# Kernel optimization log

Hardware: AMD Instinct MI355X
Metric: run time of the kernel (lower is better)

The kernel has to match this reference:

```python
import jax, jax.numpy as jnp
import numpy as np

EPS = 1e-6
BN_EPS = 1e-5


def _grid_idx(loc, Hg, Wg):
    # loc: [B, N0, 2] in [-1, 1], (x, y) order -> nearest cell index in Hg x Wg grid
    loc = jnp.clip(loc, -1.0, 1.0)
    px = jnp.clip(jnp.round(0.5 * (loc[..., 0] + 1.0) * Wg - 0.5).astype(jnp.int32), 0, Wg - 1)
    py = jnp.clip(jnp.round(0.5 * (loc[..., 1] + 1.0) * Hg - 0.5).astype(jnp.int32), 0, Hg - 1)
    return py * Wg + px  # [B, N0]


def token2map(x, loc_orig, idx_agg, H, W):
    # scatter-average token features into an H x W map via the original points
    B, N, C = x.shape
    idx_hw = _grid_idx(loc_orig, H, W)                         # [B, N0]
    feat = jnp.take_along_axis(x, idx_agg[..., None], axis=1)  # [B, N0, C]
    ssum = jax.vmap(lambda s, i, f: s.at[i].add(f))(jnp.zeros((B, H * W, C), x.dtype), idx_hw, feat)
    cnt = jax.vmap(lambda c, i: c.at[i].add(1.0))(jnp.zeros((B, H * W), x.dtype), idx_hw)
    return (ssum / (cnt[..., None] + EPS)).reshape(B, H, W, C)


def map2token(x_map, N, loc_orig, idx_agg, agg_weight):
    # bilinear gather from map at original points, then weighted scatter-mean to N tokens
    B, Hd, Wd, C = x_map.shape
    loc = jnp.clip(loc_orig, -1.0, 1.0)
    fx = jnp.clip(0.5 * (loc[..., 0] + 1.0) * Wd - 0.5, 0.0, Wd - 1.0)
    fy = jnp.clip(0.5 * (loc[..., 1] + 1.0) * Hd - 0.5, 0.0, Hd - 1.0)
    x0 = jnp.floor(fx); y0 = jnp.floor(fy)
    wx = fx - x0; wy = fy - y0
    x0i = x0.astype(jnp.int32); y0i = y0.astype(jnp.int32)
    x1i = jnp.minimum(x0i + 1, Wd - 1); y1i = jnp.minimum(y0i + 1, Hd - 1)
    mp = x_map.reshape(B, Hd * Wd, C)
    g = lambda iy, ix: jnp.take_along_axis(mp, (iy * Wd + ix)[..., None], axis=1)  # [B, N0, C]
    f = (((1 - wx) * (1 - wy))[..., None] * g(y0i, x0i)
         + (wx * (1 - wy))[..., None] * g(y0i, x1i)
         + ((1 - wx) * wy)[..., None] * g(y1i, x0i)
         + (wx * wy)[..., None] * g(y1i, x1i))
    wpt = agg_weight[..., 0]                                   # [B, N0]
    num = jax.vmap(lambda n, i, s: n.at[i].add(s))(jnp.zeros((B, N, C), f.dtype), idx_agg, f * wpt[..., None])
    den = jax.vmap(lambda d, i, w: d.at[i].add(w))(jnp.zeros((B, N), f.dtype), idx_agg, wpt)
    return num / (den[..., None] + EPS)


def token_cluster_grid(x, loc_orig, idx_agg, agg_weight, weight, Hc, Wc):
    # weighted merge of tokens into Hc x Wc coarse grid cells (keyed by original points)
    B, N, C = x.shape
    Ns = Hc * Wc
    idx_cell = _grid_idx(loc_orig, Hc, Wc)                     # [B, N0] -> new token id
    wtok = weight[..., 0]                                      # [B, N] token confidence weight
    wpt = jnp.take_along_axis(wtok, idx_agg, axis=1)           # [B, N0]
    fpt = jnp.take_along_axis(x, idx_agg[..., None], axis=1)   # [B, N0, C]
    num = jax.vmap(lambda n, i, s: n.at[i].add(s))(jnp.zeros((B, Ns, C), x.dtype), idx_cell, fpt * wpt[..., None])
    den = jax.vmap(lambda d, i, w: d.at[i].add(w))(jnp.zeros((B, Ns), x.dtype), idx_cell, wpt)
    x_down = num / (den[..., None] + EPS)
    weight_t = (wpt / (jnp.take_along_axis(den, idx_cell, axis=1) + EPS))[..., None]  # [B, N0, 1]
    agg_weight_down = agg_weight * weight_t
    agg_weight_down = agg_weight_down / jnp.max(agg_weight_down, axis=1, keepdims=True)
    return x_down, idx_cell, agg_weight_down


def setup_inputs() -> dict:
    key = jax.random.key(0)
    ks = jax.random.split(key, 8)
    B, N, C_in, C_out = 4, 16384, 128, 256
    H = W = 256
    N0 = H * W
    x = jax.random.normal(ks[0], (B, N, C_in), jnp.float32)
    loc_orig = jax.random.uniform(ks[1], (B, N0, 2), jnp.float32, -1.0, 1.0)
    idx_agg = jax.random.randint(ks[2], (B, N0), 0, N, jnp.int32)
    agg_weight = jax.random.uniform(ks[3], (B, N0, 1), jnp.float32)
    conv_w = jax.random.normal(ks[4], (3, 3, C_in, C_out), jnp.float32) / np.sqrt(9 * C_in).astype(np.float32)
    conv_b = jnp.zeros((C_out,), jnp.float32)
    skip_w = jax.random.normal(ks[5], (C_out, C_in), jnp.float32) / np.sqrt(C_in).astype(np.float32)
    bn_gamma = jnp.ones((C_out,), jnp.float32)
    bn_beta = jnp.zeros((C_out,), jnp.float32)
    conf_w = jax.random.normal(ks[6], (1, C_out), jnp.float32) / np.sqrt(C_out).astype(np.float32)
    conf_b = jnp.zeros((1,), jnp.float32)
    return {"x": x, "loc_orig": loc_orig, "idx_agg": idx_agg, "agg_weight": agg_weight,
            "conv_w": conv_w, "conv_b": conv_b, "skip_w": skip_w,
            "bn_gamma": bn_gamma, "bn_beta": bn_beta, "conf_w": conf_w, "conf_b": conf_b,
            "H": H, "W": W}


def reference(x, loc_orig, idx_agg, agg_weight, conv_w, conv_b, skip_w, bn_gamma, bn_beta, conf_w, conf_b, H, W):
    B, N, C = x.shape
    # scatter tokens to map, 3x3 s2 conv
    x_map = token2map(x, loc_orig, idx_agg, H, W)              # [B, H, W, C]
    y = jax.lax.conv_general_dilated(x_map, conv_w, (2, 2), ((1, 1), (1, 1)),
                                     dimension_numbers=("NHWC", "HWIO", "NHWC")) + conv_b
    Hd = (H - 1) // 2 + 1
    Wd = (W - 1) // 2 + 1
    # gather back to tokens + linear skip
    tok = map2token(y, N, loc_orig, idx_agg, agg_weight) + x @ skip_w.T   # [B, N, C_out]
    # BatchNorm2d over tokens (train-mode batch stats, per channel)
    mu = jnp.mean(tok, axis=(0, 1))
    var = jnp.var(tok, axis=(0, 1))
    tokn = (tok - mu) / jnp.sqrt(var + BN_EPS) * bn_gamma + bn_beta
    conf = tokn @ conf_w.T + conf_b                            # [B, N, 1]
    weight = jnp.exp(conf)
    # grid clustering: merge to (Hd//2) x (Wd//2) cells = N * sample_ratio tokens
    x_down, idx_agg_down, agg_weight_down = token_cluster_grid(tokn, loc_orig, idx_agg, agg_weight, weight, Hd // 2, Wd // 2)
    x_down = jax.nn.relu(x_down)
    x_out = jax.nn.relu(tokn)
    return x_down, x_out, conf, agg_weight_down, idx_agg_down
```

## Files before the change

kernel.cpp:

```cpp
#include <hip/hip_runtime.h>
#include <hip/hip_bf16.h>
#include <math.h>

#define BB    4
#define NTOK  16384
#define CIN   128
#define COUT  256
#define HM    256
#define WM    256
#define NP    65536
#define HD    128
#define WD    128
#define HC    64
#define WC    64
#define NS    4096
#define EPS   1e-6f
#define BNEPS 1e-5f

#define SEG_TOK  (BB * NP)
#define SEG_64   (SEG_TOK + BB * NTOK)
#define NSEG     (SEG_64 + BB * NS)

typedef __attribute__((ext_vector_type(8))) short bfrag8;
typedef __attribute__((ext_vector_type(4))) float ffrag4;

static constexpr size_t BNSUM_OFF  = 0;
static constexpr size_t BNSQ_OFF   = BNSUM_OFF + 256;
static constexpr size_t MAXW_OFF   = BNSQ_OFF + 256;
static constexpr size_t CNTS_OFF   = MAXW_OFF + 256;
static constexpr size_t CURS_OFF   = CNTS_OFF + NSEG;
static constexpr size_t ZERO_FLOATS = CURS_OFF + NSEG;
static constexpr size_t YBUF_OFF   = (ZERO_FLOATS + 255) & ~(size_t)255;
static constexpr size_t XMAPN_OFF  = YBUF_OFF + (size_t)BB * HD * WD * COUT / 2;
static constexpr size_t XBF_OFF    = XMAPN_OFF + (size_t)BB * NP * CIN / 2;
static constexpr size_t TOKB_OFF   = XBF_OFF + (size_t)BB * NTOK * CIN / 2;
static constexpr size_t WFRAG_OFF  = TOKB_OFF + (size_t)BB * NTOK * COUT / 2;
static constexpr size_t SFRAG_OFF  = WFRAG_OFF + (size_t)9 * 4 * 16 * 512 / 2;
static constexpr size_t WEXP_OFF   = SFRAG_OFF + (size_t)4 * 16 * 512 / 2;
static constexpr size_t AWDT_OFF   = WEXP_OFF + (size_t)BB * NTOK;
static constexpr size_t ABUF_OFF   = AWDT_OFF + (size_t)BB * NP;
static constexpr size_t BBUF_OFF   = ABUF_OFF + 256;
static constexpr size_t CWA_OFF    = BBUF_OFF + 256;
static constexpr size_t C0_OFF     = CWA_OFF + 256;
static constexpr size_t CELL256_OFF = C0_OFF + 256;
static constexpr size_t CELL64_OFF  = CELL256_OFF + (size_t)BB * NP;
static constexpr size_t DEN2_OFF   = CELL64_OFF + (size_t)BB * NP;
static constexpr size_t STARTS_OFF = DEN2_OFF + (size_t)BB * NS;
static constexpr size_t BLKSUM_OFF = STARTS_OFF + NSEG;
static constexpr size_t BLKEXCL_OFF = BLKSUM_OFF + 512;
static constexpr size_t PIDX_OFF   = BLKEXCL_OFF + 512;


__device__ __forceinline__ unsigned short f2bf(float f) {
    unsigned int u = __float_as_uint(f);
    return (unsigned short)((u + 0x7FFFu + ((u >> 16) & 1u)) >> 16);
}
__device__ __forceinline__ float bf2f(unsigned short u) {
    return __uint_as_float((unsigned int)u << 16);
}


__global__ void k_cellhist(const float* __restrict__ loc, const int* __restrict__ idx_agg,
                           int* __restrict__ cell256, int* __restrict__ cell64,
                           int* __restrict__ cnts) {
    int i = blockIdx.x * 256 + threadIdx.x;
    int b = i >> 16;
    float lx = fminf(fmaxf(loc[2 * (size_t)i], -1.f), 1.f);
    float ly = fminf(fmaxf(loc[2 * (size_t)i + 1], -1.f), 1.f);
    int px = (int)rintf(0.5f * (lx + 1.f) * WM - 0.5f);
    px = min(max(px, 0), WM - 1);
    int py = (int)rintf(0.5f * (ly + 1.f) * HM - 0.5f);
    py = min(max(py, 0), HM - 1);
    int c256 = py * WM + px;
    cell256[i] = c256;
    int qx = (int)rintf(0.5f * (lx + 1.f) * WC - 0.5f);
    qx = min(max(qx, 0), WC - 1);
    int qy = (int)rintf(0.5f * (ly + 1.f) * HC - 0.5f);
    qy = min(max(qy, 0), HC - 1);
    int c64 = qy * WC + qx;
    cell64[i] = c64;
    atomicAdd(&cnts[b * NP + c256], 1);
    atomicAdd(&cnts[SEG_TOK + b * NTOK + idx_agg[i]], 1);
    atomicAdd(&cnts[SEG_64 + b * NS + c64], 1);
}

__global__ void k_xcast(const float* __restrict__ x, unsigned short* __restrict__ xbf) {
    size_t i = (size_t)blockIdx.x * 256 + threadIdx.x;
    float4 v = ((const float4*)x)[i];
    ushort4 o;
    o.x = f2bf(v.x); o.y = f2bf(v.y); o.z = f2bf(v.z); o.w = f2bf(v.w);
    ((ushort4*)xbf)[i] = o;
}

__global__ __launch_bounds__(256) void k_scan1(const int* __restrict__ cnts,
                                               int* __restrict__ starts,
                                               int* __restrict__ blksum) {
    int t = threadIdx.x;
    int base = blockIdx.x * 1024 + t * 4;
    int4 v = *(const int4*)(cnts + base);
    int tsum = v.x + v.y + v.z + v.w;
    __shared__ int s[256];
    s[t] = tsum;
    __syncthreads();
    for (int off = 1; off < 256; off <<= 1) {
        int add = (t >= off) ? s[t - off] : 0;
        __syncthreads();
        s[t] += add;
        __syncthreads();
    }
    int excl = s[t] - tsum;
    int4 o;
    o.x = excl; o.y = excl + v.x; o.z = o.y + v.y; o.w = o.z + v.z;
    *(int4*)(starts + base) = o;
    if (t == 255) blksum[blockIdx.x] = s[255];
}

__global__ __launch_bounds__(512) void k_scan2(const int* __restrict__ blksum,
                                               int* __restrict__ blkexcl) {
    int t = threadIdx.x;
    __shared__ int s[512];
    int v = (t < 336) ? blksum[t] : 0;
    s[t] = v;
    __syncthreads();
    for (int off = 1; off < 512; off <<= 1) {
        int add = (t >= off) ? s[t - off] : 0;
        __syncthreads();
        s[t] += add;
        __syncthreads();
    }
    if (t < 336) blkexcl[t] = s[t] - v;
}

__global__ void k_fill(const int* __restrict__ cell256, const int* __restrict__ idx_agg,
                       const int* __restrict__ cell64, const int* __restrict__ starts,
                       const int* __restrict__ blkexcl, int* __restrict__ curs,
                       int* __restrict__ pidx) {
    int gp = blockIdx.x * 256 + threadIdx.x;
    int b = gp >> 16;
    int ia = idx_agg[gp];
    int t1 = b * NP + cell256[gp];
    int p1 = starts[t1] + blkexcl[t1 >> 10] + atomicAdd(&curs[t1], 1);
    pidx[p1] = ia;
    int t2 = SEG_TOK + b * NTOK + ia;
    int p2 = starts[t2] + blkexcl[t2 >> 10] + atomicAdd(&curs[t2], 1);
    pidx[p2] = gp;
    int t3 = SEG_64 + b * NS + cell64[gp];
    int p3 = starts[t3] + blkexcl[t3 >> 10] + atomicAdd(&curs[t3], 1);
    pidx[p3] = ia;
}

__global__ __launch_bounds__(256) void k_gather_map(const unsigned short* __restrict__ xbf,
                                                    const int* __restrict__ starts,
                                                    const int* __restrict__ blkexcl,
                                                    const int* __restrict__ cnts,
                                                    const int* __restrict__ pidx,
                                                    unsigned short* __restrict__ xmapn) {
    int tgt = blockIdx.x * 8 + (threadIdx.x >> 5);
    int lane = threadIdx.x & 31;
    int b = tgt >> 16;
    int start = starts[tgt] + blkexcl[tgt >> 10];
    int cnt = cnts[tgt];
    float4 acc = make_float4(0.f, 0.f, 0.f, 0.f);
    for (int j = 0; j < cnt; ++j) {
        int tk = pidx[start + j];
        ushort4 u = *(const ushort4*)(xbf + ((size_t)b * NTOK + tk) * CIN + lane * 4);
        acc.x += bf2f(u.x); acc.y += bf2f(u.y); acc.z += bf2f(u.z); acc.w += bf2f(u.w);
    }
    float inv = 1.0f / ((float)cnt + EPS);
    ushort4 o;
    o.x = f2bf(acc.x * inv);
    o.y = f2bf(acc.y * inv);
    o.z = f2bf(acc.z * inv);
    o.w = f2bf(acc.w * inv);
    *(ushort4*)(xmapn + (size_t)tgt * CIN + lane * 4) = o;
}

__global__ void k_wfrag(const float* __restrict__ cw, unsigned short* __restrict__ wfrag) {
    int i = blockIdx.x * 256 + threadIdx.x;
    int j = i & 7;
    int lane = (i >> 3) & 63;
    int nt = (i >> 9) & 15;
    int kc = (i >> 13) & 3;
    int khw = i >> 15;
    int c = kc * 32 + ((lane >> 4) << 3) + j;
    int n = nt * 16 + (lane & 15);
    wfrag[i] = f2bf(cw[((size_t)khw * CIN + c) * COUT + n]);
}

__global__ void k_sfrag(const float* __restrict__ sw, unsigned short* __restrict__ sfrag) {
    int i = blockIdx.x * 256 + threadIdx.x;
    int j = i & 7;
    int lane = (i >> 3) & 63;
    int nt = (i >> 9) & 15;
    int kc = i >> 13;
    int c = kc * 32 + ((lane >> 4) << 3) + j;
    int n = nt * 16 + (lane & 15);
    sfrag[i] = f2bf(sw[(size_t)n * CIN + c]);
}

__global__ __launch_bounds__(256) void k_convmf(const unsigned short* __restrict__ xmapn,
                                                const unsigned short* __restrict__ wfrag,
                                                const float* __restrict__ cb,
                                                unsigned short* __restrict__ y) {
    int bz = blockIdx.x;
    int ow0 = (bz & 1) * 64;
    int oh = (bz >> 1) & (HD - 1);
    int b = bz >> 8;
    int tid = threadIdx.x;
    int w = tid >> 6, lane = tid & 63;
    int n0 = w * 64;

    __shared__ unsigned short s_even[65 * 136];
    __shared__ unsigned short s_odd[64 * 136];

    ffrag4 acc[4][4];
#pragma unroll
    for (int mt = 0; mt < 4; ++mt)
#pragma unroll
        for (int nt = 0; nt < 4; ++nt) {
            ffrag4 z = {0.f, 0.f, 0.f, 0.f};
            acc[mt][nt] = z;
        }

    int iw0 = 2 * ow0 - 1;
    int lm = lane & 15;
    int lq = lane >> 4;
    int cbase = lq << 3;

    for (int kh = 0; kh < 3; ++kh) {
        int ih = 2 * oh - 1 + kh;
        __syncthreads();
        {
            const unsigned short* rowb =
                xmapn + ((size_t)b * NP + (size_t)ih * WM) * CIN;
            bool ihok = (ih >= 0 && ih < HM);
            for (int idx = tid; idx < 129 * 16; idx += 256) {
                int pix = idx >> 4;
                int c8 = (idx & 15) * 8;
                int iw = iw0 + pix;
                uint4 v = make_uint4(0u, 0u, 0u, 0u);
                if (ihok && iw >= 0 && iw < WM)
                    v = *(const uint4*)(rowb + (size_t)iw * CIN + c8);
                unsigned short* dst = (pix & 1)
                    ? &s_odd[(size_t)((pix - 1) >> 1) * 136 + c8]
                    : &s_even[(size_t)(pix >> 1) * 136 + c8];
                *(uint4*)dst = v;
            }
        }
        __syncthreads();
#pragma unroll
        for (int kw = 0; kw < 3; ++kw) {
            int khw = kh * 3 + kw;
#pragma unroll
            for (int kc = 0; kc < 4; ++kc) {
                int c = kc * 32 + cbase;
                bfrag8 af[4];
#pragma unroll
                for (int mt = 0; mt < 4; ++mt) {
                    int m = mt * 16 + lm;
                    const unsigned short* src;
                    if (kw == 1)      src = &s_odd[(size_t)m * 136 + c];
                    else if (kw == 0) src = &s_even[(size_t)m * 136 + c];
                    else              src = &s_even[(size_t)(m + 1) * 136 + c];
                    af[mt] = *(const bfrag8*)(const void*)src;
                }
                const unsigned short* wb =
                    wfrag + ((size_t)((khw * 4 + kc) * 16) + w * 4) * 512 + lane * 8;
#pragma unroll
                for (int nt = 0; nt < 4; ++nt) {
                    bfrag8 bf = *(const bfrag8*)(const void*)(wb + (size_t)nt * 512);
#pragma unroll
                    for (int mt = 0; mt < 4; ++mt)
                        acc[mt][nt] = __builtin_amdgcn_mfma_f32_16x16x32_bf16(
                            af[mt], bf, acc[mt][nt], 0, 0, 0);
                }
            }
        }
    }

    unsigned short* yb = y + (((size_t)b * HD + oh) * WD + ow0) * COUT;
#pragma unroll
    for (int nt = 0; nt < 4; ++nt) {
        int n = n0 + nt * 16 + lm;
        float bias = cb[n];
#pragma unroll
        for (int mt = 0; mt < 4; ++mt) {
#pragma unroll
            for (int r = 0; r < 4; ++r) {
                int m = mt * 16 + lq * 4 + r;
                yb[(size_t)m * COUT + n] = f2bf(acc[mt][nt][r] + bias);
            }
        }
    }
}

__global__ __launch_bounds__(256) void k_gtokmf(const unsigned short* __restrict__ y,
                                                const float* __restrict__ loc,
                                                const float* __restrict__ aggw,
                                                const unsigned short* __restrict__ xbf,
                                                const unsigned short* __restrict__ sfrag,
                                                const int* __restrict__ starts,
                                                const int* __restrict__ blkexcl,
                                                const int* __restrict__ cnts,
                                                const int* __restrict__ pidx,
                                                float* __restrict__ tok,
                                                float* __restrict__ bnsum,
                                                float* __restrict__ bnsq) {
    int t0 = blockIdx.x * 64;
    int tid = threadIdx.x;
    int w = tid >> 6, lane = tid & 63;
    __shared__ unsigned short s_num[64 * 264];

    for (int i = 0; i < 16; ++i) {
        int row = w * 16 + i;
        int tl = t0 + row;
        int b = tl >> 14;
        int tgt = SEG_TOK + tl;
        int start = starts[tgt] + blkexcl[tgt >> 10];
        int cnt = cnts[tgt];
        const unsigned short* ybase = y + (size_t)b * (HD * WD * COUT);
        float4 num = make_float4(0.f, 0.f, 0.f, 0.f);
        float den = 0.f;
        for (int j = 0; j < cnt; ++j) {
            int gp = pidx[start + j];
            float lx = fminf(fmaxf(loc[2 * (size_t)gp], -1.f), 1.f);
            float ly = fminf(fmaxf(loc[2 * (size_t)gp + 1], -1.f), 1.f);
            float fx = fminf(fmaxf(0.5f * (lx + 1.f) * WD - 0.5f, 0.f), (float)(WD - 1));
            float fy = fminf(fmaxf(0.5f * (ly + 1.f) * HD - 0.5f, 0.f), (float)(HD - 1));
            float x0f = floorf(fx), y0f = floorf(fy);
            float wx = fx - x0f, wy = fy - y0f;
            int x0 = (int)x0f, y0 = (int)y0f;
            int x1 = min(x0 + 1, WD - 1), y1 = min(y0 + 1, HD - 1);
            ushort4 u00 = *(const ushort4*)(ybase + ((size_t)y0 * WD + x0) * COUT + lane * 4);
            ushort4 u01 = *(const ushort4*)(ybase + ((size_t)y0 * WD + x1) * COUT + lane * 4);
            ushort4 u10 = *(const ushort4*)(ybase + ((size_t)y1 * WD + x0) * COUT + lane * 4);
            ushort4 u11 = *(const ushort4*)(ybase + ((size_t)y1 * WD + x1) * COUT + lane * 4);
            float w00 = (1.f - wx) * (1.f - wy), w01 = wx * (1.f - wy);
            float w10 = (1.f - wx) * wy, w11 = wx * wy;
            float aw = aggw[gp];
            num.x += (w00 * bf2f(u00.x) + w01 * bf2f(u01.x) + w10 * bf2f(u10.x) + w11 * bf2f(u11.x)) * aw;
            num.y += (w00 * bf2f(u00.y) + w01 * bf2f(u01.y) + w10 * bf2f(u10.y) + w11 * bf2f(u11.y)) * aw;
            num.z += (w00 * bf2f(u00.z) + w01 * bf2f(u01.z) + w10 * bf2f(u10.z) + w11 * bf2f(u11.z)) * aw;
            num.w += (w00 * bf2f(u00.w) + w01 * bf2f(u01.w) + w10 * bf2f(u10.w) + w11 * bf2f(u11.w)) * aw;
            den += aw;
        }
        float inv = 1.f / (den + EPS);
        ushort4 o;
        o.x = f2bf(num.x * inv);
        o.y = f2bf(num.y * inv);
        o.z = f2bf(num.z * inv);
        o.w = f2bf(num.w * inv);
        *(ushort4*)&s_num[(size_t)row * 264 + lane * 4] = o;
    }
    __syncthreads();

    int lm = lane & 15, lq = lane >> 4;
    int n0 = w * 64;
    ffrag4 acc[4][4];
#pragma unroll
    for (int mt = 0; mt < 4; ++mt)
#pragma unroll
        for (int nt = 0; nt < 4; ++nt) {
            ffrag4 z = {0.f, 0.f, 0.f, 0.f};
            acc[mt][nt] = z;
        }
#pragma unroll
    for (int kc = 0; kc < 4; ++kc) {
        bfrag8 af[4];
#pragma unroll
        for (int mt = 0; mt < 4; ++mt)
            af[mt] = *(const bfrag8*)(const void*)(xbf +
                     (size_t)(t0 + mt * 16 + lm) * CIN + kc * 32 + lq * 8);
        const unsigned short* sb = sfrag + ((size_t)(kc * 16) + w * 4) * 512 + lane * 8;
#pragma unroll
        for (int nt = 0; nt < 4; ++nt) {
            bfrag8 bf = *(const bfrag8*)(const void*)(sb + (size_t)nt * 512);
#pragma unroll
            for (int mt = 0; mt < 4; ++mt)
                acc[mt][nt] = __builtin_amdgcn_mfma_f32_16x16x32_bf16(
                    af[mt], bf, acc[mt][nt], 0, 0, 0);
        }
    }

    float bsum[4] = {0.f, 0.f, 0.f, 0.f};
    float bsq[4] = {0.f, 0.f, 0.f, 0.f};
#pragma unroll
    for (int mt = 0; mt < 4; ++mt) {
#pragma unroll
        for (int r = 0; r < 4; ++r) {
            int row = mt * 16 + lq * 4 + r;
            int tkn = t0 + row;
#pragma unroll
            for (int nt = 0; nt < 4; ++nt) {
                int n = n0 + nt * 16 + lm;
                float v = bf2f(s_num[(size_t)row * 264 + n]) + acc[mt][nt][r];
                tok[(size_t)tkn * COUT + n] = v;
                bsum[nt] += v;
                bsq[nt] = fmaf(v, v, bsq[nt]);
            }
        }
    }
#pragma unroll
    for (int nt = 0; nt < 4; ++nt) {
        bsum[nt] += __shfl_down(bsum[nt], 32);
        bsq[nt] += __shfl_down(bsq[nt], 32);
        bsum[nt] += __shfl_down(bsum[nt], 16);
        bsq[nt] += __shfl_down(bsq[nt], 16);
    }
    if (lq == 0) {
#pragma unroll
        for (int nt = 0; nt < 4; ++nt) {
            int n = n0 + nt * 16 + lm;
            atomicAdd(&bnsum[n], bsum[nt]);
            atomicAdd(&bnsq[n], bsq[nt]);
        }
    }
}

__global__ void k_bnparams(const float* __restrict__ bnsum, const float* __restrict__ bnsq,
                           const float* __restrict__ gamma, const float* __restrict__ beta,
                           const float* __restrict__ confw, const float* __restrict__ confb,
                           float* __restrict__ abuf, float* __restrict__ bbuf,
                           float* __restrict__ cwa, float* __restrict__ c0) {
    int k = threadIdx.x;
    const float cntv = (float)(BB * NTOK);
    float mu = bnsum[k] / cntv;
    float var = bnsq[k] / cntv - mu * mu;
    float a = gamma[k] * rsqrtf(var + BNEPS);
    float bbv = beta[k] - mu * a;
    abuf[k] = a;
    bbuf[k] = bbv;
    float cw = confw[k];
    cwa[k] = a * cw;
    __shared__ float red[256];
    red[k] = bbv * cw;
    __syncthreads();
    for (int s = 128; s > 0; s >>= 1) {
        if (k < s) red[k] += red[k + s];
        __syncthreads();
    }
    if (k == 0) c0[0] = red[0] + confb[0];
}

__global__ void k_confrelu(float* __restrict__ tok, const float* __restrict__ cwa,
                           const float* __restrict__ c0v, const float* __restrict__ abuf,
                           const float* __restrict__ bbuf, float* __restrict__ conf_out,
                           unsigned short* __restrict__ tokb, float* __restrict__ wexp) {
    int tid = threadIdx.x;
    int tkn = blockIdx.x * 16 + (tid >> 4);
    int kc = (tid & 15) * 16;
    float* row = tok + (size_t)tkn * COUT + kc;
    unsigned short* tb = tokb + (size_t)tkn * COUT + kc;
    float s = 0.f;
#pragma unroll
    for (int i = 0; i < 16; i += 4) {
        float4 v = *(const float4*)(row + i);
        float4 w = *(const float4*)(cwa + kc + i);
        float4 a = *(const float4*)(abuf + kc + i);
        float4 bb = *(const float4*)(bbuf + kc + i);
        s += v.x * w.x + v.y * w.y + v.z * w.z + v.w * w.w;
        float4 tn;
        tn.x = fmaf(a.x, v.x, bb.x);
        tn.y = fmaf(a.y, v.y, bb.y);
        tn.z = fmaf(a.z, v.z, bb.z);
        tn.w = fmaf(a.w, v.w, bb.w);
        ushort4 o;
        o.x = f2bf(tn.x); o.y = f2bf(tn.y); o.z = f2bf(tn.z); o.w = f2bf(tn.w);
        *(ushort4*)(tb + i) = o;
        float4 rl;
        rl.x = fmaxf(tn.x, 0.f); rl.y = fmaxf(tn.y, 0.f);
        rl.z = fmaxf(tn.z, 0.f); rl.w = fmaxf(tn.w, 0.f);
        *(float4*)(row + i) = rl;
    }
    for (int off = 8; off > 0; off >>= 1) s += __shfl_down(s, off, 16);
    if ((tid & 15) == 0) {
        float cv = s + c0v[0];
        conf_out[tkn] = cv;
        wexp[tkn] = expf(cv);
    }
}

__global__ __launch_bounds__(256) void k_gather_cluster(const unsigned short* __restrict__ tokb,
                                                        const float* __restrict__ wexp,
                                                        const int* __restrict__ starts,
                                                        const int* __restrict__ blkexcl,
                                                        const int* __restrict__ cnts,
                                                        const int* __restrict__ pidx,
                                                        float* __restrict__ xdown,
                                                        float* __restrict__ den2) {
    int wv = threadIdx.x >> 6, lane = threadIdx.x & 63;
    int tl = blockIdx.x * 4 + wv;
    int b = tl >> 12;
    int tgt = SEG_64 + tl;
    int start = starts[tgt] + blkexcl[tgt >> 10];
    int cnt = cnts[tgt];
    float4 num = make_float4(0.f, 0.f, 0.f, 0.f);
    float den = 0.f;
    for (int j = 0; j < cnt; ++j) {
        int ia = pidx[start + j];
        float w = wexp[(size_t)b * NTOK + ia];
        ushort4 u = *(const ushort4*)(tokb + ((size_t)b * NTOK + ia) * COUT + lane * 4);
        num.x = fmaf(bf2f(u.x), w, num.x);
        num.y = fmaf(bf2f(u.y), w, num.y);
        num.z = fmaf(bf2f(u.z), w, num.z);
        num.w = fmaf(bf2f(u.w), w, num.w);
        den += w;
    }
    float inv = 1.f / (den + EPS);
    float4 o;
    o.x = fmaxf(num.x * inv, 0.f);
    o.y = fmaxf(num.y * inv, 0.f);
    o.z = fmaxf(num.z * inv, 0.f);
    o.w = fmaxf(num.w * inv, 0.f);
    *(float4*)(xdown + (size_t)tl * COUT + lane * 4) = o;
    if (lane == 0) den2[tl] = den;
}

__global__ void k_awd1(const float* __restrict__ wexp, const float* __restrict__ den2,
                       const int* __restrict__ idx_agg, const int* __restrict__ cell64,
                       const float* __restrict__ aggw, float* __restrict__ awdt,
                       float* __restrict__ idx_out_f, unsigned int* __restrict__ maxw) {
    int b = blockIdx.x >> 6;
    int chunk = blockIdx.x & 63;
    int base = b * NP + chunk * 1024;
    float lmax = 0.f;
    for (int t = threadIdx.x; t < 1024; t += 256) {
        int gp = base + t;
        int ia = idx_agg[gp];
        int cell = cell64[gp];
        float w = wexp[(size_t)b * NTOK + ia];
        float wt = w / (den2[(size_t)b * NS + cell] + EPS);
        float tv = aggw[gp] * wt;
        awdt[gp] = tv;
        idx_out_f[gp] = (float)cell;
        lmax = fmaxf(lmax, tv);
    }
    __shared__ float red[256];
    red[threadIdx.x] = lmax;
    __syncthreads();
    for (int s = 128; s > 0; s >>= 1) {
        if (threadIdx.x < s) red[threadIdx.x] = fmaxf(red[threadIdx.x], red[threadIdx.x + s]);
        __syncthreads();
    }
    if (threadIdx.x == 0) atomicMax(maxw + b, __float_as_uint(red[0]));
}

__global__ void k_awd2(const float* __restrict__ awdt, const unsigned int* __restrict__ maxw,
                       float* __restrict__ awd_out) {
    int i = blockIdx.x * 256 + threadIdx.x;
    int b = i >> 16;
    awd_out[i] = awdt[i] / __uint_as_float(maxw[b]);
}

extern "C" void kernel_launch(void* const* d_in, const int* in_sizes, int n_in,
                              void* d_out, int out_size, void* d_ws, size_t ws_size,
                              hipStream_t stream) {
    const float* x        = (const float*)d_in[0];
    const float* loc      = (const float*)d_in[1];
    const int*   idx_agg  = (const int*)d_in[2];
    const float* aggw     = (const float*)d_in[3];
    const float* conv_w   = (const float*)d_in[4];
    const float* conv_b   = (const float*)d_in[5];
    const float* skip_w   = (const float*)d_in[6];
    const float* bn_gamma = (const float*)d_in[7];
    const float* bn_beta  = (const float*)d_in[8];
    const float* conf_w   = (const float*)d_in[9];
    const float* conf_b   = (const float*)d_in[10];

    float* ws      = (float*)d_ws;
    float* bnsum   = ws + BNSUM_OFF;
    float* bnsq    = ws + BNSQ_OFF;
    unsigned int* maxw = (unsigned int*)(ws + MAXW_OFF);
    int*   cnts    = (int*)(ws + CNTS_OFF);
    int*   curs    = (int*)(ws + CURS_OFF);
    unsigned short* ybuf  = (unsigned short*)(ws + YBUF_OFF);
    unsigned short* xmapn = (unsigned short*)(ws + XMAPN_OFF);
    unsigned short* xbf   = (unsigned short*)(ws + XBF_OFF);
    unsigned short* tokb  = (unsigned short*)(ws + TOKB_OFF);
    unsigned short* wfrag = (unsigned short*)(ws + WFRAG_OFF);
    unsigned short* sfrag = (unsigned short*)(ws + SFRAG_OFF);
    float* wexp    = ws + WEXP_OFF;
    float* awdt    = ws + AWDT_OFF;
    float* abuf    = ws + ABUF_OFF;
    float* bbuf    = ws + BBUF_OFF;
    float* cwa     = ws + CWA_OFF;
    float* c0      = ws + C0_OFF;
    int*   cell256 = (int*)(ws + CELL256_OFF);
    int*   cell64  = (int*)(ws + CELL64_OFF);
    float* den2    = ws + DEN2_OFF;
    int*   starts  = (int*)(ws + STARTS_OFF);
    int*   blksum  = (int*)(ws + BLKSUM_OFF);
    int*   blkexcl = (int*)(ws + BLKEXCL_OFF);
    int*   pidx    = (int*)(ws + PIDX_OFF);

    float* out       = (float*)d_out;
    float* out_xdown = out;
    float* out_x     = out + (size_t)BB * NS * COUT;
    float* out_conf  = out_x + (size_t)BB * NTOK * COUT;
    float* out_awd   = out_conf + (size_t)BB * NTOK;
    float* out_idx   = out_awd + (size_t)BB * NP;

    hipMemsetAsync(d_ws, 0, ZERO_FLOATS * sizeof(float), stream);

    k_xcast<<<BB * NTOK * CIN / 4 / 256, 256, 0, stream>>>(x, xbf);
    k_wfrag<<<9 * 4 * 16 * 512 / 256, 256, 0, stream>>>(conv_w, wfrag);
    k_sfrag<<<4 * 16 * 512 / 256, 256, 0, stream>>>(skip_w, sfrag);
    k_cellhist<<<BB * NP / 256, 256, 0, stream>>>(loc, idx_agg, cell256, cell64, cnts);
    k_scan1<<<NSEG / 1024, 256, 0, stream>>>(cnts, starts, blksum);
    k_scan2<<<1, 512, 0, stream>>>(blksum, blkexcl);
    k_fill<<<BB * NP / 256, 256, 0, stream>>>(cell256, idx_agg, cell64, starts,
                                              blkexcl, curs, pidx);
    k_gather_map<<<BB * NP / 8, 256, 0, stream>>>(xbf, starts, blkexcl, cnts, pidx, xmapn);
    k_convmf<<<BB * HD * 2, 256, 0, stream>>>(xmapn, wfrag, conv_b, ybuf);
    k_gtokmf<<<BB * NTOK / 64, 256, 0, stream>>>(ybuf, loc, aggw, xbf, sfrag,
                                                 starts, blkexcl, cnts, pidx,
                                                 out_x, bnsum, bnsq);
    k_bnparams<<<1, 256, 0, stream>>>(bnsum, bnsq, bn_gamma, bn_beta, conf_w, conf_b,
                                      abuf, bbuf, cwa, c0);
    k_confrelu<<<BB * NTOK / 16, 256, 0, stream>>>(out_x, cwa, c0, abuf, bbuf,
                                                   out_conf, tokb, wexp);
    k_gather_cluster<<<BB * NS / 4, 256, 0, stream>>>(tokb, wexp, starts, blkexcl,
                                                      cnts, pidx, out_xdown, den2);
    k_awd1<<<BB * 64, 256, 0, stream>>>(wexp, den2, idx_agg, cell64, aggw,
                                        awdt, out_idx, maxw);
    k_awd2<<<BB * NP / 256, 256, 0, stream>>>(awdt, maxw, out_awd);
}
```

Baseline: 592.9 us.

## Split fused token gather and skip GEMM into separate kernels

Splits the fused bilinear-gather plus skip-GEMM kernel in two. The first kernel assigns one wave per token, giving far more blocks for the irregular gather, and writes the unnormalised fp32 numerator to the output buffer along with a per-token denominator. The second kernel stages x tiles in LDS, runs the MFMA skip matmul, and adds the normalised numerator read back from global memory. This exposes more parallelism and latency hiding in the gather, at the cost of an extra fp32 round trip through global memory and one more launch. The numerator now stays fp32 rather than being rounded to bf16, which slightly changes numerics.

```diff
diff --git a/kernel.cpp b/kernel.cpp
--- a/kernel.cpp
+++ b/kernel.cpp
@@ -44,7 +44,8 @@
 static constexpr size_t C0_OFF     = CWA_OFF + 256;
 static constexpr size_t CELL256_OFF = C0_OFF + 256;
 static constexpr size_t CELL64_OFF  = CELL256_OFF + (size_t)BB * NP;
-static constexpr size_t DEN2_OFF   = CELL64_OFF + (size_t)BB * NP;
+static constexpr size_t DEN1_OFF   = CELL64_OFF + (size_t)BB * NP;
+static constexpr size_t DEN2_OFF   = DEN1_OFF + (size_t)BB * NTOK;
 static constexpr size_t STARTS_OFF = DEN2_OFF + (size_t)BB * NS;
 static constexpr size_t BLKSUM_OFF = STARTS_OFF + NSEG;
 static constexpr size_t BLKEXCL_OFF = BLKSUM_OFF + 512;
@@ -294,68 +295,71 @@
     }
 }
 
-__global__ __launch_bounds__(256) void k_gtokmf(const unsigned short* __restrict__ y,
-                                                const float* __restrict__ loc,
-                                                const float* __restrict__ aggw,
-                                                const unsigned short* __restrict__ xbf,
-                                                const unsigned short* __restrict__ sfrag,
-                                                const int* __restrict__ starts,
-                                                const int* __restrict__ blkexcl,
-                                                const int* __restrict__ cnts,
-                                                const int* __restrict__ pidx,
-                                                float* __restrict__ tok,
-                                                float* __restrict__ bnsum,
-                                                float* __restrict__ bnsq) {
+__global__ __launch_bounds__(256) void k_gather_tok(const unsigned short* __restrict__ y,
+                                                    const float* __restrict__ loc,
+                                                    const float* __restrict__ aggw,
+                                                    const int* __restrict__ starts,
+                                                    const int* __restrict__ blkexcl,
+                                                    const int* __restrict__ cnts,
+                                                    const int* __restrict__ pidx,
+                                                    float* __restrict__ num_out,
+                                                    float* __restrict__ den1) {
+    int wv = threadIdx.x >> 6, lane = threadIdx.x & 63;
+    int tl = blockIdx.x * 4 + wv;
+    int b = tl >> 14;
+    int tgt = SEG_TOK + tl;
+    int start = starts[tgt] + blkexcl[tgt >> 10];
+    int cnt = cnts[tgt];
+    const unsigned short* ybase = y + (size_t)b * (HD * WD * COUT);
+    float4 num = make_float4(0.f, 0.f, 0.f, 0.f);
+    float den = 0.f;
+    for (int j = 0; j < cnt; ++j) {
+        int gp = pidx[start + j];
+        float lx = fminf(fmaxf(loc[2 * (size_t)gp], -1.f), 1.f);
+        float ly = fminf(fmaxf(loc[2 * (size_t)gp + 1], -1.f), 1.f);
+        float fx = fminf(fmaxf(0.5f * (lx + 1.f) * WD - 0.5f, 0.f), (float)(WD - 1));
+        float fy = fminf(fmaxf(0.5f * (ly + 1.f) * HD - 0.5f, 0.f), (float)(HD - 1));
+        float x0f = floorf(fx), y0f = floorf(fy);
+        float wx = fx - x0f, wy = fy - y0f;
+        int x0 = (int)x0f, y0 = (int)y0f;
+        int x1 = min(x0 + 1, WD - 1), y1 = min(y0 + 1, HD - 1);
+        ushort4 u00 = *(const ushort4*)(ybase + ((size_t)y0 * WD + x0) * COUT + lane * 4);
+        ushort4 u01 = *(const ushort4*)(ybase + ((size_t)y0 * WD + x1) * COUT + lane * 4);
+        ushort4 u10 = *(const ushort4*)(ybase + ((size_t)y1 * WD + x0) * COUT + lane * 4);
+        ushort4 u11 = *(const ushort4*)(ybase + ((size_t)y1 * WD + x1) * COUT + lane * 4);
+        float w00 = (1.f - wx) * (1.f - wy), w01 = wx * (1.f - wy);
+        float w10 = (1.f - wx) * wy, w11 = wx * wy;
+        float aw = aggw[gp];
+        num.x += (w00 * bf2f(u00.x) + w01 * bf2f(u01.x) + w10 * bf2f(u10.x) + w11 * bf2f(u11.x)) * aw;
+        num.y += (w00 * bf2f(u00.y) + w01 * bf2f(u01.y) + w10 * bf2f(u10.y) + w11 * bf2f(u11.y)) * aw;
+        num.z += (w00 * bf2f(u00.z) + w01 * bf2f(u01.z) + w10 * bf2f(u10.z) + w11 * bf2f(u11.z)) * aw;
+        num.w += (w00 * bf2f(u00.w) + w01 * bf2f(u01.w) + w10 * bf2f(u10.w) + w11 * bf2f(u11.w)) * aw;
+        den += aw;
+    }
+    *(float4*)(num_out + (size_t)tl * COUT + lane * 4) = num;
+    if (lane == 0) den1[tl] = den;
+}
+
+__global__ __launch_bounds__(256) void k_tokmf(const unsigned short* __restrict__ xbf,
+                                               const unsigned short* __restrict__ sfrag,
+                                               const float* __restrict__ den1,
+                                               float* __restrict__ tok,
+                                               float* __restrict__ bnsum,
+                                               float* __restrict__ bnsq) {
     int t0 = blockIdx.x * 64;
     int tid = threadIdx.x;
     int w = tid >> 6, lane = tid & 63;
-    __shared__ unsigned short s_num[64 * 264];
-
-    for (int i = 0; i < 16; ++i) {
-        int row = w * 16 + i;
-        int tl = t0 + row;
-        int b = tl >> 14;
-        int tgt = SEG_TOK + tl;
-        int start = starts[tgt] + blkexcl[tgt >> 10];
-        int cnt = cnts[tgt];
-        const unsigned short* ybase = y + (size_t)b * (HD * WD * COUT);
-        float4 num = make_float4(0.f, 0.f, 0.f, 0.f);
-        float den = 0.f;
-        for (int j = 0; j < cnt; ++j) {
-            int gp = pidx[start + j];
-            float lx = fminf(fmaxf(loc[2 * (size_t)gp], -1.f), 1.f);
-            float ly = fminf(fmaxf(loc[2 * (size_t)gp + 1], -1.f), 1.f);
-            float fx = fminf(fmaxf(0.5f * (lx + 1.f) * WD - 0.5f, 0.f), (float)(WD - 1));
-            float fy = fminf(fmaxf(0.5f * (ly + 1.f) * HD - 0.5f, 0.f), (float)(HD - 1));
-            float x0f = floorf(fx), y0f = floorf(fy);
-            float wx = fx - x0f, wy = fy - y0f;
-            int x0 = (int)x0f, y0 = (int)y0f;
-            int x1 = min(x0 + 1, WD - 1), y1 = min(y0 + 1, HD - 1);
-            ushort4 u00 = *(const ushort4*)(ybase + ((size_t)y0 * WD + x0) * COUT + lane * 4);
-            ushort4 u01 = *(const ushort4*)(ybase + ((size_t)y0 * WD + x1) * COUT + lane * 4);
-            ushort4 u10 = *(const ushort4*)(ybase + ((size_t)y1 * WD + x0) * COUT + lane * 4);
-            ushort4 u11 = *(const ushort4*)(ybase + ((size_t)y1 * WD + x1) * COUT + lane * 4);
-            float w00 = (1.f - wx) * (1.f - wy), w01 = wx * (1.f - wy);
-            float w10 = (1.f - wx) * wy, w11 = wx * wy;
-            float aw = aggw[gp];
-            num.x += (w00 * bf2f(u00.x) + w01 * bf2f(u01.x) + w10 * bf2f(u10.x) + w11 * bf2f(u11.x)) * aw;
-            num.y += (w00 * bf2f(u00.y) + w01 * bf2f(u01.y) + w10 * bf2f(u10.y) + w11 * bf2f(u11.y)) * aw;
-            num.z += (w00 * bf2f(u00.z) + w01 * bf2f(u01.z) + w10 * bf2f(u10.z) + w11 * bf2f(u11.z)) * aw;
-            num.w += (w00 * bf2f(u00.w) + w01 * bf2f(u01.w) + w10 * bf2f(u10.w) + w11 * bf2f(u11.w)) * aw;
-            den += aw;
-        }
-        float inv = 1.f / (den + EPS);
-        ushort4 o;
-        o.x = f2bf(num.x * inv);
-        o.y = f2bf(num.y * inv);
-        o.z = f2bf(num.z * inv);
-        o.w = f2bf(num.w * inv);
-        *(ushort4*)&s_num[(size_t)row * 264 + lane * 4] = o;
+    int n0 = w * 64;
+    int lm = lane & 15, lq = lane >> 4;
+
+    __shared__ unsigned short s_x[64 * 136];
+    const unsigned short* xb = xbf + (size_t)t0 * CIN;
+    for (int idx = tid; idx < 64 * 16; idx += 256) {
+        int row = idx >> 4, c8 = (idx & 15) * 8;
+        *(uint4*)&s_x[(size_t)row * 136 + c8] = *(const uint4*)(xb + (size_t)row * CIN + c8);
     }
     __syncthreads();
 
-    int lm = lane & 15, lq = lane >> 4;
-    int n0 = w * 64;
     ffrag4 acc[4][4];
 #pragma unroll
     for (int mt = 0; mt < 4; ++mt)
@@ -364,13 +368,14 @@
             ffrag4 z = {0.f, 0.f, 0.f, 0.f};
             acc[mt][nt] = z;
         }
+
 #pragma unroll
     for (int kc = 0; kc < 4; ++kc) {
+        int c = kc * 32 + lq * 8;
         bfrag8 af[4];
 #pragma unroll
         for (int mt = 0; mt < 4; ++mt)
-            af[mt] = *(const bfrag8*)(const void*)(xbf +
-                     (size_t)(t0 + mt * 16 + lm) * CIN + kc * 32 + lq * 8);
+            af[mt] = *(const bfrag8*)(const void*)&s_x[(size_t)(mt * 16 + lm) * 136 + c];
         const unsigned short* sb = sfrag + ((size_t)(kc * 16) + w * 4) * 512 + lane * 8;
 #pragma unroll
         for (int nt = 0; nt < 4; ++nt) {
@@ -388,13 +393,14 @@
     for (int mt = 0; mt < 4; ++mt) {
 #pragma unroll
         for (int r = 0; r < 4; ++r) {
-            int row = mt * 16 + lq * 4 + r;
-            int tkn = t0 + row;
+            int tkn = t0 + mt * 16 + lq * 4 + r;
+            float inv = 1.f / (den1[tkn] + EPS);
 #pragma unroll
             for (int nt = 0; nt < 4; ++nt) {
                 int n = n0 + nt * 16 + lm;
-                float v = bf2f(s_num[(size_t)row * 264 + n]) + acc[mt][nt][r];
-                tok[(size_t)tkn * COUT + n] = v;
+                size_t a = (size_t)tkn * COUT + n;
+                float v = tok[a] * inv + acc[mt][nt][r];
+                tok[a] = v;
                 bsum[nt] += v;
                 bsq[nt] = fmaf(v, v, bsq[nt]);
             }
@@ -587,6 +593,7 @@
     float* c0      = ws + C0_OFF;
     int*   cell256 = (int*)(ws + CELL256_OFF);
     int*   cell64  = (int*)(ws + CELL64_OFF);
+    float* den1    = ws + DEN1_OFF;
     float* den2    = ws + DEN2_OFF;
     int*   starts  = (int*)(ws + STARTS_OFF);
     int*   blksum  = (int*)(ws + BLKSUM_OFF);
@@ -612,9 +619,9 @@
                                               blkexcl, curs, pidx);
     k_gather_map<<<BB * NP / 8, 256, 0, stream>>>(xbf, starts, blkexcl, cnts, pidx, xmapn);
     k_convmf<<<BB * HD * 2, 256, 0, stream>>>(xmapn, wfrag, conv_b, ybuf);
-    k_gtokmf<<<BB * NTOK / 64, 256, 0, stream>>>(ybuf, loc, aggw, xbf, sfrag,
-                                                 starts, blkexcl, cnts, pidx,
-                                                 out_x, bnsum, bnsq);
+    k_gather_tok<<<BB * NTOK / 4, 256, 0, stream>>>(ybuf, loc, aggw, starts, blkexcl,
+                                                    cnts, pidx, out_x, den1);
+    k_tokmf<<<BB * NTOK / 64, 256, 0, stream>>>(xbf, sfrag, den1, out_x, bnsum, bnsq);
     k_bnparams<<<1, 256, 0, stream>>>(bnsum, bnsq, bn_gamma, bn_beta, conf_w, conf_b,
                                       abuf, bbuf, cwa, c0);
     k_confrelu<<<BB * NTOK / 16, 256, 0, stream>>>(out_x, cwa, c0, abuf, bbuf,
```

Result: faster. 549.1 us (-7.4%).
